# Kernel tuning notes

Measured on AMD Instinct MI355X. Metric: run time of the kernel, lower is better.

Reference implementation:

```python
import jax, jax.numpy as jnp
import numpy as np

S, B, HID, NH = 256, 2, 512, 8
HD = HID // NH
C = 1.0            # Poincare ball curvature c (geoopt k = -c)
SQC = C ** 0.5
EPS = 1e-15


def _artanh(x):
    return jnp.arctanh(jnp.clip(x, -1 + 1e-7, 1 - 1e-7))


def artan_k(x):
    return _artanh(SQC * x) / SQC


def tan_k(x):
    return jnp.tanh(SQC * x) / SQC


def mobius_add(x, y):
    x2 = jnp.sum(x * x, -1, keepdims=True)
    y2 = jnp.sum(y * y, -1, keepdims=True)
    xy = jnp.sum(x * y, -1, keepdims=True)
    num = (1 + 2 * C * xy + C * y2) * x + (1 - C * x2) * y
    den = 1 + 2 * C * xy + C * C * x2 * y2
    return num / jnp.maximum(den, EPS)


def mobius_matvec(W, x):
    x_norm = jnp.maximum(jnp.linalg.norm(x, axis=-1, keepdims=True), EPS)
    mx = x @ W.T
    mx_norm = jnp.maximum(jnp.linalg.norm(mx, axis=-1, keepdims=True), EPS)
    res = tan_k(mx_norm / x_norm * artan_k(x_norm)) * (mx / mx_norm)
    zero = jnp.all(mx == 0, axis=-1, keepdims=True)
    return jnp.where(zero, 0.0, res)


def projx(x):
    n = jnp.maximum(jnp.linalg.norm(x, axis=-1, keepdims=True), EPS)
    maxnorm = (1 - 4e-3) / SQC  # float32 eps in geoopt
    return jnp.where(n > maxnorm, x / n * maxnorm, x)


def expmap0(u):
    n = jnp.maximum(jnp.linalg.norm(u, axis=-1, keepdims=True), EPS)
    return tan_k(n) * u / n


def logmap0(y):
    n = jnp.maximum(jnp.linalg.norm(y, axis=-1, keepdims=True), EPS)
    return artan_k(n) * y / n


def mobius_scalar_mul(r, x):
    n = jnp.maximum(jnp.linalg.norm(x, axis=-1, keepdims=True), EPS)
    return tan_k(r * artan_k(n)) * x / n


def manifold_linear(W, b, x):
    return projx(mobius_add(mobius_matvec(W, x), b))


def setup_inputs() -> dict:
    key = jax.random.key(0)
    ks = jax.random.split(key, 7)
    q = jax.random.normal(ks[0], (S, B, HID), jnp.float32) * 0.02
    w = lambda k: jax.random.normal(k, (HID, HID), jnp.float32) * 0.02
    bias = lambda k: jax.random.normal(k, (HID,), jnp.float32) * 0.01
    return {"query": q,
            "Wq": w(ks[1]), "bq": bias(ks[2]),
            "Wk": w(ks[3]), "bk": bias(ks[4]),
            "Wv": w(ks[5]), "bv": bias(ks[6])}


def reference(query, Wq, bq, Wk, bk, Wv, bv):
    x = jnp.transpose(query, (1, 0, 2))  # [B,S,HID], key=value=query
    Bn, Sn, _ = x.shape
    q = manifold_linear(Wq, bq, x)
    k = manifold_linear(Wk, bk, x)
    v = manifold_linear(Wv, bv, x)
    # faithful to torch .view(-1, H, S, D): plain memory reshape (not transpose)
    ql = expmap0(logmap0(q).reshape(Bn, NH, Sn, HD))
    kl = expmap0(logmap0(k).reshape(Bn, NH, Sn, HD))
    vl = expmap0(logmap0(v).reshape(Bn, NH, Sn, HD))
    # pairwise mobius_add(-q, k) -> [B,H,Q,N,D]; torch norm(p=-2) over D (faithful)
    diff = mobius_add(-ql[:, :, :, None, :], kl[:, :, None, :, :])
    t1 = jnp.sum(jnp.maximum(diff * diff, 1e-30) ** -1.0, axis=-1) ** -0.5
    scores = jnp.clip(-2.0 * artan_k(t1), -1e10, 1e10)
    probs = jax.nn.sigmoid(scores)  # [B,H,Q,N]; dropout p=0 -> identity
    # weighted gyro-midpoint over N (geoopt _weighted_midpoint, reducedim=[-1])
    gamma = 2.0 / jnp.maximum(1.0 - C * jnp.sum(vl * vl, -1), EPS)  # [B,H,N]
    denom = jnp.einsum('bhqn,bhn->bhq', probs, gamma - 1.0)
    sgn = jnp.where(denom >= 0, 1.0, -1.0)
    denom = sgn * jnp.maximum(jnp.abs(denom), 1e-10)
    nom = jnp.einsum('bhqn,bhnd->bhqd', probs, gamma[..., None] * vl)
    ctx = mobius_scalar_mul(0.5, nom / denom[..., None])  # [B,H,Q,D]
    ctx = jnp.transpose(ctx, (0, 2, 1, 3))  # [B,Q,H,D]
    ctx = expmap0(logmap0(ctx).reshape(Bn, Sn, HID))
    return jnp.transpose(ctx, (1, 0, 2)), probs
```

## Files before the change

### kernel.cpp

```cpp
#include <hip/hip_runtime.h>
#include <math.h>

constexpr int S_   = 256;
constexpr int B_   = 2;
constexpr int HID_ = 512;
constexpr int NH_  = 8;
constexpr int HD_  = 64;
constexpr int BSH  = B_ * S_ * HID_;

__device__ __forceinline__ float artanh_c(float x) {
    x = fminf(fmaxf(x, -0.9999999f), 0.9999999f);
    return 0.5f * __logf((1.f + x) / (1.f - x));
}

__device__ __forceinline__ float wsum64(float v) {
    #pragma unroll
    for (int o = 1; o < 64; o <<= 1) v += __shfl_xor(v, o, 64);
    return v;
}

__device__ __forceinline__ float block_sum_256(float v, float* red) {
    const int t = threadIdx.x;
    __syncthreads();
    red[t] = v;
    __syncthreads();
    #pragma unroll
    for (int sft = 128; sft > 0; sft >>= 1) {
        if (t < sft) red[t] += red[t + sft];
        __syncthreads();
    }
    return red[0];
}

__global__ __launch_bounds__(256) void gemm3_kernel(
    const float* __restrict__ query,
    const float* __restrict__ Wq, const float* __restrict__ Wk,
    const float* __restrict__ Wv, float* __restrict__ ws_mx)
{
    const int tid   = threadIdx.x;
    const int which = blockIdx.x >> 8;
    const int tmp   = blockIdx.x & 255;
    const int row0  = (tmp >> 4) * 32;
    const int col0  = (tmp & 15) * 32;
    const float* __restrict__ W = (which == 0) ? Wq : (which == 1) ? Wk : Wv;
    float* __restrict__ outp = ws_mx + (size_t)which * (HID_ * HID_);

    __shared__ __align__(16) float sA[32][36];
    __shared__ __align__(16) float sB[32][36];

    const int sr = tid >> 3;
    const int sk = (tid & 7) * 4;
    const int gra = row0 + sr;
    const float* pa = query + (size_t)((gra & 255) * 2 + (gra >> 8)) * HID_ + sk;
    const float* pb = W + (size_t)(col0 + sr) * HID_ + sk;

    const int ty = tid >> 4, tx = tid & 15;
    float acc[2][2] = {};

    float4 va = *(const float4*)pa;
    float4 vb = *(const float4*)pb;
    for (int k0 = 0; k0 < HID_; k0 += 32) {
        __syncthreads();
        sA[sk+0][sr] = va.x; sA[sk+1][sr] = va.y; sA[sk+2][sr] = va.z; sA[sk+3][sr] = va.w;
        sB[sk+0][sr] = vb.x; sB[sk+1][sr] = vb.y; sB[sk+2][sr] = vb.z; sB[sk+3][sr] = vb.w;
        __syncthreads();
        if (k0 + 32 < HID_) {
            va = *(const float4*)(pa + k0 + 32);
            vb = *(const float4*)(pb + k0 + 32);
        }
        #pragma unroll
        for (int kk = 0; kk < 32; ++kk) {
            const float2 av = *(const float2*)&sA[kk][ty * 2];
            const float2 bv = *(const float2*)&sB[kk][tx * 2];
            acc[0][0] = fmaf(av.x, bv.x, acc[0][0]);
            acc[0][1] = fmaf(av.x, bv.y, acc[0][1]);
            acc[1][0] = fmaf(av.y, bv.x, acc[1][0]);
            acc[1][1] = fmaf(av.y, bv.y, acc[1][1]);
        }
    }
    #pragma unroll
    for (int i = 0; i < 2; ++i) {
        *(float2*)&outp[(size_t)(row0 + ty * 2 + i) * HID_ + col0 + tx * 2] =
            make_float2(acc[i][0], acc[i][1]);
    }
}

__global__ __launch_bounds__(256) void mobius_rows_kernel(
    const float* __restrict__ query,
    const float* __restrict__ bq, const float* __restrict__ bk,
    const float* __restrict__ bv,
    float* __restrict__ ws_qkv, float* __restrict__ ws_gamma)
{
    const int lane = threadIdx.x & 63;
    const int wv   = threadIdx.x >> 6;
    const int row  = blockIdx.x * 4 + wv;
    const int which = row >> 9;
    const int rr    = row & 511;
    const float* __restrict__ bias = (which == 0) ? bq : (which == 1) ? bk : bv;
    float* mrow = ws_qkv + (size_t)row * HID_;
    const float* xrow = query + (size_t)((rr & 255) * 2 + (rr >> 8)) * HID_;

    float m[8], x[8], bb[8];
    *(float4*)&m[0]  = ((const float4*)mrow)[lane * 2];
    *(float4*)&m[4]  = ((const float4*)mrow)[lane * 2 + 1];
    *(float4*)&x[0]  = ((const float4*)xrow)[lane * 2];
    *(float4*)&x[4]  = ((const float4*)xrow)[lane * 2 + 1];
    *(float4*)&bb[0] = ((const float4*)bias)[lane * 2];
    *(float4*)&bb[4] = ((const float4*)bias)[lane * 2 + 1];

    float x2p = 0.f, m2p = 0.f, b2p = 0.f;
    #pragma unroll
    for (int j = 0; j < 8; ++j) {
        x2p = fmaf(x[j], x[j], x2p);
        m2p = fmaf(m[j], m[j], m2p);
        b2p = fmaf(bb[j], bb[j], b2p);
    }
    const float x2s = wsum64(x2p);
    const float mn2 = wsum64(m2p);
    const float b2s = wsum64(b2p);
    const float xn = fmaxf(sqrtf(x2s), 1e-15f);
    const float mn = fmaxf(sqrtf(mn2), 1e-15f);
    const float fac = tanhf(mn / xn * artanh_c(xn)) / mn;
    float r[8];
    float r2p = 0.f, ryp = 0.f;
    #pragma unroll
    for (int j = 0; j < 8; ++j) {
        r[j] = fac * m[j];
        r2p = fmaf(r[j], r[j], r2p);
        ryp = fmaf(r[j], bb[j], ryp);
    }
    const float r2s = wsum64(r2p);
    const float ry  = wsum64(ryp);
    const float a_c = 1.f + 2.f * ry + b2s;
    const float b_c = 1.f - r2s;
    const float den = 1.f + 2.f * ry + r2s * b2s;
    const float inv_den = 1.f / fmaxf(den, 1e-15f);
    float h[8];
    float h2p = 0.f;
    #pragma unroll
    for (int j = 0; j < 8; ++j) {
        h[j] = (a_c * r[j] + b_c * bb[j]) * inv_den;
        h2p = fmaf(h[j], h[j], h2p);
    }
    const float h2s = wsum64(h2p);
    float hn = fmaxf(sqrtf(h2s), 1e-15f);
    float pf = 1.f;
    if (hn > 0.996f) { pf = 0.996f / hn; hn = 0.996f; }
    const float lf = artanh_c(hn) / hn * pf;
    float l[8];
    float l2p = 0.f;
    #pragma unroll
    for (int j = 0; j < 8; ++j) {
        l[j] = lf * h[j];
        l2p = fmaf(l[j], l[j], l2p);
    }
    float cs = l2p;
    cs += __shfl_xor(cs, 1, 64);
    cs += __shfl_xor(cs, 2, 64);
    cs += __shfl_xor(cs, 4, 64);
    const float cn = fmaxf(sqrtf(cs), 1e-15f);
    const float th = tanhf(cn);
    const float sc = th / cn;
    float o[8];
    #pragma unroll
    for (int j = 0; j < 8; ++j) o[j] = sc * l[j];
    ((float4*)mrow)[lane * 2]     = *(float4*)&o[0];
    ((float4*)mrow)[lane * 2 + 1] = *(float4*)&o[4];
    if (which == 2 && (lane & 7) == 0) {
        const int j = lane >> 3;
        ws_gamma[(size_t)rr * NH_ + j] = 2.f / fmaxf(1.f - th * th, 1e-15f);
    }
}

__global__ __launch_bounds__(256) void attn_kernel(
    const float* __restrict__ ws_qkv, const float* __restrict__ gamma,
    float* __restrict__ probs, float* __restrict__ lc)
{
    const int tid = threadIdx.x;
    const int bh  = blockIdx.x >> 5;
    const int q0  = (blockIdx.x & 31) * 8;
    const float* __restrict__ ql = ws_qkv + (size_t)bh * (S_ * HD_);
    const float* __restrict__ kl = ws_qkv + (size_t)BSH + (size_t)bh * (S_ * HD_);
    const float* __restrict__ vl = ws_qkv + (size_t)2 * BSH + (size_t)bh * (S_ * HD_);

    __shared__ __align__(16) float kS[128 * 64];
    __shared__ __align__(16) float qS[8 * 64];
    __shared__ __align__(16) float pS[8 * 256];
    __shared__ float gS[S_];
    __shared__ float k2S[128];
    __shared__ float nomP[4][8][64];
    __shared__ float dnS[8];

    gS[tid] = gamma[(size_t)bh * S_ + tid];
    if (tid < 128) ((float4*)qS)[tid] = ((const float4*)(ql + (size_t)q0 * 64))[tid];
    __syncthreads();

    const int q_l = tid >> 5;
    const int n_i = tid & 31;
    float qv[64];
    #pragma unroll
    for (int c = 0; c < 16; ++c)
        *(float4*)&qv[c * 4] = *(const float4*)&qS[q_l * 64 + c * 4];
    float q2 = 0.f;
    #pragma unroll
    for (int d = 0; d < 64; ++d) q2 = fmaf(qv[d], qv[d], q2);
    const float b_c = 1.f - q2;
    float* __restrict__ prow = probs + ((size_t)(bh * S_ + q0 + q_l)) * S_;

    const int c4 = tid & 15;
    const int nb = tid >> 4;
    float sp = 0.f, spg = 0.f;

    for (int half = 0; half < 2; ++half) {
        __syncthreads();
        #pragma unroll
        for (int jj = 0; jj < 8; ++jj) {
            const int n = nb + 16 * jj;
            const float4 v = *(const float4*)(kl + ((size_t)(half * 128 + n)) * 64 + c4 * 4);
            *(float4*)&kS[n * 64 + ((c4 ^ (n & 15)) * 4)] = v;
            float pk = fmaf(v.x, v.x, fmaf(v.y, v.y, fmaf(v.z, v.z, v.w * v.w)));
            pk += __shfl_xor(pk, 1, 64);
            pk += __shfl_xor(pk, 2, 64);
            pk += __shfl_xor(pk, 4, 64);
            pk += __shfl_xor(pk, 8, 64);
            if (c4 == 0) k2S[n] = pk;
        }
        __syncthreads();
        #pragma unroll
        for (int j = 0; j < 4; ++j) {
            const int n = n_i + 32 * j;
            float kv[64];
            #pragma unroll
            for (int c = 0; c < 16; ++c)
                *(float4*)&kv[c * 4] = *(const float4*)&kS[n * 64 + ((c ^ (n & 15)) * 4)];
            float s = 0.f;
            #pragma unroll
            for (int d = 0; d < 64; ++d) s = fmaf(qv[d], kv[d], s);
            const float k2  = k2S[n];
            const float a_c = 1.f - 2.f * s + k2;
            const float den = fmaxf(fmaf(q2, k2, 1.f - 2.f * s), 1e-15f);
            const float ra  = __builtin_amdgcn_rcpf(a_c);
            const float r_c = b_c * ra;
            const float scale = den * den * ra * ra;
            const float c2  = 1e-30f * scale;
            float invsum = 0.f;
            #pragma unroll
            for (int d = 0; d < 64; ++d) {
                const float w = fmaf(r_c, kv[d], -qv[d]);
                invsum += __builtin_amdgcn_rcpf(fmaf(w, w, c2));
            }
            const float t1 = __builtin_amdgcn_rsqf(scale * invsum);
            const float p = 0.5f - 0.5f * fminf(t1, 0.9999999f);
            const int gn = half * 128 + n;
            prow[gn] = p;
            const float g = gS[gn];
            pS[q_l * 256 + gn] = p * g;
            sp += p; spg += p * g;
        }
    }
    #pragma unroll
    for (int o = 1; o < 32; o <<= 1) {
        sp  += __shfl_xor(sp, o, 64);
        spg += __shfl_xor(spg, o, 64);
    }
    if ((tid & 31) == 0) dnS[q_l] = spg - sp;
    __syncthreads();

    const int w = tid >> 6, d = tid & 63;
    float acc[8] = {};
    const float* __restrict__ vbase = vl + (size_t)(w * 64) * 64;
    #pragma unroll 4
    for (int i4 = 0; i4 < 16; ++i4) {
        float vv[4];
        #pragma unroll
        for (int j2 = 0; j2 < 4; ++j2) vv[j2] = vbase[(size_t)(i4 * 4 + j2) * 64 + d];
        #pragma unroll
        for (int qq = 0; qq < 8; ++qq) {
            const float4 pq = *(const float4*)&pS[qq * 256 + w * 64 + i4 * 4];
            acc[qq] = fmaf(pq.x, vv[0], acc[qq]);
            acc[qq] = fmaf(pq.y, vv[1], acc[qq]);
            acc[qq] = fmaf(pq.z, vv[2], acc[qq]);
            acc[qq] = fmaf(pq.w, vv[3], acc[qq]);
        }
    }
    #pragma unroll
    for (int qq = 0; qq < 8; ++qq) nomP[w][qq][d] = acc[qq];
    __syncthreads();

    #pragma unroll
    for (int t = 0; t < 2; ++t) {
        const int qq = (tid >> 6) + 4 * t;
        const float nom = nomP[0][qq][d] + nomP[1][qq][d] + nomP[2][qq][d] + nomP[3][qq][d];
        const float dd = dnS[qq];
        const float adn = fmaxf(fabsf(dd), 1e-10f);
        const float sden = (dd >= 0.f) ? adn : -adn;
        const float m = nom / sden;
        const float ss = wsum64(m * m);
        const float nn = fmaxf(sqrtf(ss), 1e-15f);
        const float s1 = tanhf(0.5f * artanh_c(nn));
        const float res = s1 * m / nn;
        const float nres = fmaxf(s1, 1e-15f);
        lc[((size_t)(bh * S_ + q0 + qq)) * HD_ + d] = (artanh_c(nres) / nres) * res;
    }
}

__global__ __launch_bounds__(256) void outproj_kernel(
    const float* __restrict__ lc, float* __restrict__ out0)
{
    const int t = threadIdx.x;
    const int s = blockIdx.x & (S_ - 1);
    const int b = blockIdx.x >> 8;
    __shared__ float red[256];
    const int h0 = t >> 6, d0 = t & 63;
    const int e1 = t + 256;
    const int h1 = e1 >> 6, d1 = e1 & 63;
    const float v0 = lc[(((size_t)(b * NH_ + h0)) * S_ + s) * HD_ + d0];
    const float v1 = lc[(((size_t)(b * NH_ + h1)) * S_ + s) * HD_ + d1];
    const float ss = block_sum_256(v0 * v0 + v1 * v1, red);
    const float nn = fmaxf(sqrtf(ss), 1e-15f);
    const float f = tanhf(nn) / nn;
    float* orow = out0 + ((size_t)(s * B_ + b)) * HID_;
    orow[t] = f * v0;
    orow[t + 256] = f * v1;
}

extern "C" void kernel_launch(void* const* d_in, const int* in_sizes, int n_in,
                              void* d_out, int out_size, void* d_ws, size_t ws_size,
                              hipStream_t stream) {
    (void)in_sizes; (void)n_in; (void)out_size; (void)ws_size;
    const float* query = (const float*)d_in[0];
    const float* Wq = (const float*)d_in[1];
    const float* bq = (const float*)d_in[2];
    const float* Wk = (const float*)d_in[3];
    const float* bk = (const float*)d_in[4];
    const float* Wv = (const float*)d_in[5];
    const float* bv = (const float*)d_in[6];

    float* out0  = (float*)d_out;
    float* probs = out0 + (size_t)S_ * B_ * HID_;

    float* ws       = (float*)d_ws;
    float* ws_qkv   = ws;
    float* ws_gamma = ws + (size_t)3 * BSH;
    float* ws_lc    = ws + (size_t)3 * BSH + 4096;

    gemm3_kernel<<<dim3(768), dim3(256), 0, stream>>>(query, Wq, Wk, Wv, ws_qkv);
    mobius_rows_kernel<<<dim3(384), dim3(256), 0, stream>>>(query, bq, bk, bv, ws_qkv, ws_gamma);
    attn_kernel<<<dim3(512), dim3(256), 0, stream>>>(ws_qkv, ws_gamma, probs, ws_lc);
    outproj_kernel<<<dim3(B_ * S_), dim3(256), 0, stream>>>(ws_lc, out0);
}
```

Measured before the change: 129.0 us.

## Restructure QKV GEMM with wave-uniform A loads and swizzled W tile

Rewrites the projection GEMM so each block computes a 32x128 output tile. Each wave holds 8 rows whose query values are read straight from global memory as wave-uniform (broadcast) loads, and each lane computes two output columns from an XOR-swizzled shared-memory W tile. The aim is fewer, larger blocks with more work per thread and fewer shared-memory transactions. The costs are that A is no longer staged in LDS, so each k-step issues scalar or broadcast global loads, and only 192 blocks are launched, which may leave many CUs on the MI355X idle.

```diff
diff --git a/kernel.cpp b/kernel.cpp
--- a/kernel.cpp
+++ b/kernel.cpp
@@ -37,51 +37,65 @@
     const float* __restrict__ Wq, const float* __restrict__ Wk,
     const float* __restrict__ Wv, float* __restrict__ ws_mx)
 {
-    const int tid   = threadIdx.x;
-    const int which = blockIdx.x >> 8;
-    const int tmp   = blockIdx.x & 255;
-    const int row0  = (tmp >> 4) * 32;
-    const int col0  = (tmp & 15) * 32;
+    const int tid  = threadIdx.x;
+    const int lane = tid & 63;
+    const int wv   = __builtin_amdgcn_readfirstlane(tid >> 6);
+    const int rb   = blockIdx.x >> 2;
+    const int cb   = (blockIdx.x & 3) * 128;
+    const int which = (rb * 32) >> 9;
     const float* __restrict__ W = (which == 0) ? Wq : (which == 1) ? Wk : Wv;
-    float* __restrict__ outp = ws_mx + (size_t)which * (HID_ * HID_);
-
-    __shared__ __align__(16) float sA[32][36];
-    __shared__ __align__(16) float sB[32][36];
-
-    const int sr = tid >> 3;
-    const int sk = (tid & 7) * 4;
-    const int gra = row0 + sr;
-    const float* pa = query + (size_t)((gra & 255) * 2 + (gra >> 8)) * HID_ + sk;
-    const float* pb = W + (size_t)(col0 + sr) * HID_ + sk;
-
-    const int ty = tid >> 4, tx = tid & 15;
-    float acc[2][2] = {};
-
-    float4 va = *(const float4*)pa;
-    float4 vb = *(const float4*)pb;
+
+    const int rloc = (rb * 32) & 511;
+    const int wrow = rloc + wv * 8;
+    const float* xr[8];
+    #pragma unroll
+    for (int i = 0; i < 8; ++i) {
+        const int rr = wrow + i;
+        xr[i] = query + (size_t)((rr & 255) * 2 + (rr >> 8)) * HID_;
+    }
+
+    __shared__ __align__(16) float sB[128 * 32];
+
+    const int sc = tid >> 1;
+    const int sk = (tid & 1) * 16;
+    const float* wp = W + (size_t)(cb + sc) * HID_ + sk;
+    const int swz_st = (sc & 7) << 2;
+
+    float acc[8][2] = {};
+    float4 bvp[4];
+    #pragma unroll
+    for (int j = 0; j < 4; ++j) bvp[j] = *(const float4*)(wp + j * 4);
+
     for (int k0 = 0; k0 < HID_; k0 += 32) {
         __syncthreads();
-        sA[sk+0][sr] = va.x; sA[sk+1][sr] = va.y; sA[sk+2][sr] = va.z; sA[sk+3][sr] = va.w;
-        sB[sk+0][sr] = vb.x; sB[sk+1][sr] = vb.y; sB[sk+2][sr] = vb.z; sB[sk+3][sr] = vb.w;
+        #pragma unroll
+        for (int j = 0; j < 4; ++j)
+            *(float4*)&sB[(sc * 32 + sk + j * 4) ^ swz_st] = bvp[j];
         __syncthreads();
         if (k0 + 32 < HID_) {
-            va = *(const float4*)(pa + k0 + 32);
-            vb = *(const float4*)(pb + k0 + 32);
-        }
-        #pragma unroll
-        for (int kk = 0; kk < 32; ++kk) {
-            const float2 av = *(const float2*)&sA[kk][ty * 2];
-            const float2 bv = *(const float2*)&sB[kk][tx * 2];
-            acc[0][0] = fmaf(av.x, bv.x, acc[0][0]);
-            acc[0][1] = fmaf(av.x, bv.y, acc[0][1]);
-            acc[1][0] = fmaf(av.y, bv.x, acc[1][0]);
-            acc[1][1] = fmaf(av.y, bv.y, acc[1][1]);
-        }
-    }
-    #pragma unroll
-    for (int i = 0; i < 2; ++i) {
-        *(float2*)&outp[(size_t)(row0 + ty * 2 + i) * HID_ + col0 + tx * 2] =
-            make_float2(acc[i][0], acc[i][1]);
+            #pragma unroll
+            for (int j = 0; j < 4; ++j) bvp[j] = *(const float4*)(wp + k0 + 32 + j * 4);
+        }
+        #pragma unroll
+        for (int kk = 0; kk < 32; kk += 4) {
+            const int bidx = (lane * 32 + kk) ^ ((lane & 7) << 2);
+            const float4 b0 = *(const float4*)&sB[bidx];
+            const float4 b1 = *(const float4*)&sB[bidx + 2048];
+            #pragma unroll
+            for (int i = 0; i < 8; ++i) {
+                const float4 a = *(const float4*)(xr[i] + k0 + kk);
+                acc[i][0] = fmaf(a.w, b0.w, fmaf(a.z, b0.z,
+                            fmaf(a.y, b0.y, fmaf(a.x, b0.x, acc[i][0]))));
+                acc[i][1] = fmaf(a.w, b1.w, fmaf(a.z, b1.z,
+                            fmaf(a.y, b1.y, fmaf(a.x, b1.x, acc[i][1]))));
+            }
+        }
+    }
+    #pragma unroll
+    for (int i = 0; i < 8; ++i) {
+        const size_t gr = (size_t)(rb * 32 + wv * 8 + i);
+        ws_mx[gr * HID_ + cb + lane]      = acc[i][0];
+        ws_mx[gr * HID_ + cb + 64 + lane] = acc[i][1];
     }
 }
 
@@ -344,7 +358,7 @@
     float* ws_gamma = ws + (size_t)3 * BSH;
     float* ws_lc    = ws + (size_t)3 * BSH + 4096;
 
-    gemm3_kernel<<<dim3(768), dim3(256), 0, stream>>>(query, Wq, Wk, Wv, ws_qkv);
+    gemm3_kernel<<<dim3(192), dim3(256), 0, stream>>>(query, Wq, Wk, Wv, ws_qkv);
     mobius_rows_kernel<<<dim3(384), dim3(256), 0, stream>>>(query, bq, bk, bv, ws_qkv, ws_gamma);
     attn_kernel<<<dim3(512), dim3(256), 0, stream>>>(ws_qkv, ws_gamma, probs, ws_lc);
     outproj_kernel<<<dim3(B_ * S_), dim3(256), 0, stream>>>(ws_lc, out0);
```

Result: slower. 176.3 us (+36.7%).

## Replace FP32 SIMT QKV GEMM with split-bf16 MFMA GEMM plus conversion pass

Applied to the files above, without the earlier changes.

Adds a conversion kernel that splits the query and weight matrices into high and low bf16 halves. The three projection GEMMs then run on bf16 MFMA instructions, using three products (hi*hi, hi*lo, lo*hi) to approximate FP32 accuracy. LDS tiles use an XOR swizzle. The goal is to cut the cost of the scalar FMA GEMM, in exchange for an extra kernel launch, an extra global round trip for the converted operands, and slightly lower precision than true FP32.

```diff
diff --git a/kernel.cpp b/kernel.cpp
--- a/kernel.cpp
+++ b/kernel.cpp
@@ -8,6 +8,10 @@
 constexpr int HD_  = 64;
 constexpr int BSH  = B_ * S_ * HID_;
 
+typedef unsigned short u16;
+typedef short s16x8 __attribute__((ext_vector_type(8)));
+typedef float f32x4 __attribute__((ext_vector_type(4)));
+
 __device__ __forceinline__ float artanh_c(float x) {
     x = fminf(fmaxf(x, -0.9999999f), 0.9999999f);
     return 0.5f * __logf((1.f + x) / (1.f - x));
@@ -32,57 +36,129 @@
     return red[0];
 }
 
-__global__ __launch_bounds__(256) void gemm3_kernel(
-    const float* __restrict__ query,
-    const float* __restrict__ Wq, const float* __restrict__ Wk,
-    const float* __restrict__ Wv, float* __restrict__ ws_mx)
+__global__ __launch_bounds__(256) void cvt_kernel(
+    const float* __restrict__ query, const float* __restrict__ Wq,
+    const float* __restrict__ Wk, const float* __restrict__ Wv,
+    u16* __restrict__ Ahi, u16* __restrict__ Alo,
+    u16* __restrict__ Bhi, u16* __restrict__ Blo)
 {
-    const int tid   = threadIdx.x;
-    const int which = blockIdx.x >> 8;
-    const int tmp   = blockIdx.x & 255;
-    const int row0  = (tmp >> 4) * 32;
-    const int col0  = (tmp & 15) * 32;
-    const float* __restrict__ W = (which == 0) ? Wq : (which == 1) ? Wk : Wv;
-    float* __restrict__ outp = ws_mx + (size_t)which * (HID_ * HID_);
-
-    __shared__ __align__(16) float sA[32][36];
-    __shared__ __align__(16) float sB[32][36];
-
-    const int sr = tid >> 3;
-    const int sk = (tid & 7) * 4;
-    const int gra = row0 + sr;
-    const float* pa = query + (size_t)((gra & 255) * 2 + (gra >> 8)) * HID_ + sk;
-    const float* pb = W + (size_t)(col0 + sr) * HID_ + sk;
-
-    const int ty = tid >> 4, tx = tid & 15;
-    float acc[2][2] = {};
-
-    float4 va = *(const float4*)pa;
-    float4 vb = *(const float4*)pb;
+    const int lane = threadIdx.x & 63;
+    const int gr = blockIdx.x * 4 + (threadIdx.x >> 6);
+    const float* src;
+    u16 *dh, *dl;
+    if (gr < 512) {
+        src = query + (size_t)((gr & 255) * 2 + (gr >> 8)) * HID_;
+        dh = Ahi + (size_t)gr * HID_;
+        dl = Alo + (size_t)gr * HID_;
+    } else {
+        const int m = gr - 512;
+        const float* __restrict__ W = ((m >> 9) == 0) ? Wq : ((m >> 9) == 1) ? Wk : Wv;
+        src = W + (size_t)(m & 511) * HID_;
+        dh = Bhi + (size_t)m * HID_;
+        dl = Blo + (size_t)m * HID_;
+    }
+    float v[8];
+    *(float4*)&v[0] = *(const float4*)(src + lane * 8);
+    *(float4*)&v[4] = *(const float4*)(src + lane * 8 + 4);
+    s16x8 hv, lv;
+    #pragma unroll
+    for (int j = 0; j < 8; ++j) {
+        const unsigned u = __float_as_uint(v[j]);
+        const float hf = __uint_as_float(u & 0xFFFF0000u);
+        hv[j] = (short)(u >> 16);
+        lv[j] = (short)(__float_as_uint(v[j] - hf) >> 16);
+    }
+    *(s16x8*)(dh + lane * 8) = hv;
+    *(s16x8*)(dl + lane * 8) = lv;
+}
+
+__global__ __launch_bounds__(256) void gemm3_mfma_kernel(
+    const u16* __restrict__ Ahi, const u16* __restrict__ Alo,
+    const u16* __restrict__ Bhi, const u16* __restrict__ Blo,
+    float* __restrict__ ws_mx)
+{
+    const int tid = threadIdx.x;
+    const int rt = blockIdx.x >> 3;
+    const int ct = blockIdx.x & 7;
+    const int rloc  = (rt & 7) * 64;
+    const int brow0 = (rt >> 3) * 512 + ct * 64;
+
+    __shared__ __align__(16) u16 sAh[64 * 32];
+    __shared__ __align__(16) u16 sAl[64 * 32];
+    __shared__ __align__(16) u16 sBh[64 * 32];
+    __shared__ __align__(16) u16 sBl[64 * 32];
+
+    const int r = tid >> 2, s = tid & 3;
+    const u16* gAh = Ahi + (size_t)(rloc + r) * HID_ + s * 8;
+    const u16* gAl = Alo + (size_t)(rloc + r) * HID_ + s * 8;
+    const u16* gBh = Bhi + (size_t)(brow0 + r) * HID_ + s * 8;
+    const u16* gBl = Blo + (size_t)(brow0 + r) * HID_ + s * 8;
+    const int wslot = r * 32 + ((s ^ ((r >> 1) & 3)) * 8);
+
+    const int lane = tid & 63, w = tid >> 6;
+    const int wr = w >> 1, wc = w & 1;
+    const int fr = lane & 15;
+    const int fs = lane >> 4;
+    int aslot[2], bslot[2];
+    #pragma unroll
+    for (int i = 0; i < 2; ++i) {
+        const int ar = wr * 32 + i * 16 + fr;
+        aslot[i] = ar * 32 + ((fs ^ ((ar >> 1) & 3)) * 8);
+        const int br = wc * 32 + i * 16 + fr;
+        bslot[i] = br * 32 + ((fs ^ ((br >> 1) & 3)) * 8);
+    }
+
+    f32x4 acc[2][2];
+    #pragma unroll
+    for (int i = 0; i < 2; ++i)
+        #pragma unroll
+        for (int j = 0; j < 2; ++j) acc[i][j] = (f32x4){0.f, 0.f, 0.f, 0.f};
+
+    s16x8 pf0 = *(const s16x8*)gAh;
+    s16x8 pf1 = *(const s16x8*)gAl;
+    s16x8 pf2 = *(const s16x8*)gBh;
+    s16x8 pf3 = *(const s16x8*)gBl;
+
     for (int k0 = 0; k0 < HID_; k0 += 32) {
         __syncthreads();
-        sA[sk+0][sr] = va.x; sA[sk+1][sr] = va.y; sA[sk+2][sr] = va.z; sA[sk+3][sr] = va.w;
-        sB[sk+0][sr] = vb.x; sB[sk+1][sr] = vb.y; sB[sk+2][sr] = vb.z; sB[sk+3][sr] = vb.w;
+        *(s16x8*)&sAh[wslot] = pf0;
+        *(s16x8*)&sAl[wslot] = pf1;
+        *(s16x8*)&sBh[wslot] = pf2;
+        *(s16x8*)&sBl[wslot] = pf3;
         __syncthreads();
         if (k0 + 32 < HID_) {
-            va = *(const float4*)(pa + k0 + 32);
-            vb = *(const float4*)(pb + k0 + 32);
+            pf0 = *(const s16x8*)(gAh + k0 + 32);
+            pf1 = *(const s16x8*)(gAl + k0 + 32);
+            pf2 = *(const s16x8*)(gBh + k0 + 32);
+            pf3 = *(const s16x8*)(gBl + k0 + 32);
         }
-        #pragma unroll
-        for (int kk = 0; kk < 32; ++kk) {
-            const float2 av = *(const float2*)&sA[kk][ty * 2];
-            const float2 bv = *(const float2*)&sB[kk][tx * 2];
-            acc[0][0] = fmaf(av.x, bv.x, acc[0][0]);
-            acc[0][1] = fmaf(av.x, bv.y, acc[0][1]);
-            acc[1][0] = fmaf(av.y, bv.x, acc[1][0]);
-            acc[1][1] = fmaf(av.y, bv.y, acc[1][1]);
+        s16x8 ah[2], al[2], bh[2], bl[2];
+        #pragma unroll
+        for (int i = 0; i < 2; ++i) {
+            ah[i] = *(const s16x8*)&sAh[aslot[i]];
+            al[i] = *(const s16x8*)&sAl[aslot[i]];
+            bh[i] = *(const s16x8*)&sBh[bslot[i]];
+            bl[i] = *(const s16x8*)&sBl[bslot[i]];
         }
-    }
-    #pragma unroll
-    for (int i = 0; i < 2; ++i) {
-        *(float2*)&outp[(size_t)(row0 + ty * 2 + i) * HID_ + col0 + tx * 2] =
-            make_float2(acc[i][0], acc[i][1]);
-    }
+        #pragma unroll
+        for (int i = 0; i < 2; ++i)
+            #pragma unroll
+            for (int j = 0; j < 2; ++j) {
+                acc[i][j] = __builtin_amdgcn_mfma_f32_16x16x32_bf16(ah[i], bh[j], acc[i][j], 0, 0, 0);
+                acc[i][j] = __builtin_amdgcn_mfma_f32_16x16x32_bf16(ah[i], bl[j], acc[i][j], 0, 0, 0);
+                acc[i][j] = __builtin_amdgcn_mfma_f32_16x16x32_bf16(al[i], bh[j], acc[i][j], 0, 0, 0);
+            }
+    }
+    #pragma unroll
+    for (int i = 0; i < 2; ++i)
+        #pragma unroll
+        for (int j = 0; j < 2; ++j)
+            #pragma unroll
+            for (int q = 0; q < 4; ++q) {
+                const int row = rt * 64 + wr * 32 + i * 16 + fs * 4 + q;
+                const int col = ct * 64 + wc * 32 + j * 16 + fr;
+                ws_mx[(size_t)row * HID_ + col] = acc[i][j][q];
+            }
 }
 
 __global__ __launch_bounds__(256) void mobius_rows_kernel(
@@ -343,8 +419,13 @@
     float* ws_qkv   = ws;
     float* ws_gamma = ws + (size_t)3 * BSH;
     float* ws_lc    = ws + (size_t)3 * BSH + 4096;
-
-    gemm3_kernel<<<dim3(768), dim3(256), 0, stream>>>(query, Wq, Wk, Wv, ws_qkv);
+    u16* Ahi = (u16*)(ws + (size_t)3 * BSH + 4096 + 131072);
+    u16* Alo = Ahi + (size_t)512 * HID_;
+    u16* Bhi = Alo + (size_t)512 * HID_;
+    u16* Blo = Bhi + (size_t)1536 * HID_;
+
+    cvt_kernel<<<dim3(512), dim3(256), 0, stream>>>(query, Wq, Wk, Wv, Ahi, Alo, Bhi, Blo);
+    gemm3_mfma_kernel<<<dim3(192), dim3(256), 0, stream>>>(Ahi, Alo, Bhi, Blo, ws_qkv);
     mobius_rows_kernel<<<dim3(384), dim3(256), 0, stream>>>(query, bq, bk, bv, ws_qkv, ws_gamma);
     attn_kernel<<<dim3(512), dim3(256), 0, stream>>>(ws_qkv, ws_gamma, probs, ws_lc);
     outproj_kernel<<<dim3(B_ * S_), dim3(256), 0, stream>>>(ws_lc, out0);
```

After: 110.7 us. 1.16x faster.

## Use split-bf16 MFMA for the QKV projection GEMM with swizzled double-buffered LDS

Applied to the files above, without the earlier changes.

Replaces the scalar FP32 FMA tiled GEMM for the three projections with a matrix-core version. Each fp32 operand is split into bf16 hi and lo parts, and three MFMA 16x16x32 products (hh, hl, lh) are accumulated to approximate fp32 accuracy. The kernel also uses 32x64 tiles with XOR-swizzled double-buffered LDS and register prefetch. This trades some precision (the lo*lo term is dropped) and extra split work for much higher matrix throughput, and it halves the block count.

```diff
diff --git a/kernel.cpp b/kernel.cpp
--- a/kernel.cpp
+++ b/kernel.cpp
@@ -8,6 +8,10 @@
 constexpr int HD_  = 64;
 constexpr int BSH  = B_ * S_ * HID_;
 
+typedef unsigned short u16;
+typedef short s16x8 __attribute__((ext_vector_type(8)));
+typedef float f32x4 __attribute__((ext_vector_type(4)));
+
 __device__ __forceinline__ float artanh_c(float x) {
     x = fminf(fmaxf(x, -0.9999999f), 0.9999999f);
     return 0.5f * __logf((1.f + x) / (1.f - x));
@@ -32,57 +36,103 @@
     return red[0];
 }
 
-__global__ __launch_bounds__(256) void gemm3_kernel(
+__device__ __forceinline__ void split8(const float* v, s16x8& hi, s16x8& lo) {
+    #pragma unroll
+    for (int j = 0; j < 8; ++j) {
+        const unsigned u = __float_as_uint(v[j]);
+        const float hf = __uint_as_float(u & 0xFFFF0000u);
+        hi[j] = (short)(u >> 16);
+        lo[j] = (short)(__float_as_uint(v[j] - hf) >> 16);
+    }
+}
+
+__global__ __launch_bounds__(256) void gemm3_fused_kernel(
     const float* __restrict__ query,
     const float* __restrict__ Wq, const float* __restrict__ Wk,
     const float* __restrict__ Wv, float* __restrict__ ws_mx)
 {
-    const int tid   = threadIdx.x;
-    const int which = blockIdx.x >> 8;
-    const int tmp   = blockIdx.x & 255;
-    const int row0  = (tmp >> 4) * 32;
-    const int col0  = (tmp & 15) * 32;
+    const int tid = threadIdx.x;
+    const int rt = blockIdx.x >> 3;
+    const int ct = blockIdx.x & 7;
+    const int which = (rt * 32) >> 9;
+    const int rloc  = (rt * 32) & 511;
     const float* __restrict__ W = (which == 0) ? Wq : (which == 1) ? Wk : Wv;
-    float* __restrict__ outp = ws_mx + (size_t)which * (HID_ * HID_);
-
-    __shared__ __align__(16) float sA[32][36];
-    __shared__ __align__(16) float sB[32][36];
-
-    const int sr = tid >> 3;
-    const int sk = (tid & 7) * 4;
-    const int gra = row0 + sr;
-    const float* pa = query + (size_t)((gra & 255) * 2 + (gra >> 8)) * HID_ + sk;
-    const float* pb = W + (size_t)(col0 + sr) * HID_ + sk;
-
-    const int ty = tid >> 4, tx = tid & 15;
-    float acc[2][2] = {};
-
-    float4 va = *(const float4*)pa;
-    float4 vb = *(const float4*)pb;
-    for (int k0 = 0; k0 < HID_; k0 += 32) {
+
+    __shared__ __align__(16) u16 sA[2][2][32 * 64];
+    __shared__ __align__(16) u16 sB[2][2][64 * 64];
+
+    const int ra = tid >> 3, sa = tid & 7;
+    const int rb = tid >> 2, hb = (tid & 3) * 2;
+    const int axrow = rloc + ra;
+    const float* gA = query + (size_t)((axrow & 255) * 2 + (axrow >> 8)) * HID_ + sa * 8;
+    const float* gB = W + (size_t)(ct * 64 + rb) * HID_ + hb * 8;
+    const int wA  = ra * 64 + ((sa ^ (ra & 7)) * 8);
+    const int wB0 = rb * 64 + ((hb ^ (rb & 7)) * 8);
+    const int wB1 = rb * 64 + (((hb + 1) ^ (rb & 7)) * 8);
+
+    const int lane = tid & 63, wv = tid >> 6;
+    const int fr = lane & 15, fs = lane >> 4;
+    const int aB0 = fr * 64,        ax0 = fr & 7;
+    const int aB1 = (16 + fr) * 64, ax1 = (16 + fr) & 7;
+    const int bB  = (wv * 16 + fr) * 64, bx = (wv * 16 + fr) & 7;
+
+    float a8[8], b16[16];
+    f32x4 acc[2] = {(f32x4){0.f,0.f,0.f,0.f}, (f32x4){0.f,0.f,0.f,0.f}};
+
+#define G3_LOAD(c)  do { \
+        const int k0 = (c) * 64; \
+        *(float4*)&a8[0]  = *(const float4*)(gA + k0); \
+        *(float4*)&a8[4]  = *(const float4*)(gA + k0 + 4); \
+        *(float4*)&b16[0] = *(const float4*)(gB + k0); \
+        *(float4*)&b16[4] = *(const float4*)(gB + k0 + 4); \
+        *(float4*)&b16[8] = *(const float4*)(gB + k0 + 8); \
+        *(float4*)&b16[12]= *(const float4*)(gB + k0 + 12); \
+    } while (0)
+
+#define G3_WRITE(b) do { \
+        s16x8 h_, l_; \
+        split8(a8, h_, l_); \
+        *(s16x8*)&sA[b][0][wA] = h_;  *(s16x8*)&sA[b][1][wA] = l_; \
+        split8(&b16[0], h_, l_); \
+        *(s16x8*)&sB[b][0][wB0] = h_; *(s16x8*)&sB[b][1][wB0] = l_; \
+        split8(&b16[8], h_, l_); \
+        *(s16x8*)&sB[b][0][wB1] = h_; *(s16x8*)&sB[b][1][wB1] = l_; \
+    } while (0)
+
+    G3_LOAD(0);
+    G3_WRITE(0);
+
+    for (int c = 0; c < 8; ++c) {
+        const int p = c & 1;
         __syncthreads();
-        sA[sk+0][sr] = va.x; sA[sk+1][sr] = va.y; sA[sk+2][sr] = va.z; sA[sk+3][sr] = va.w;
-        sB[sk+0][sr] = vb.x; sB[sk+1][sr] = vb.y; sB[sk+2][sr] = vb.z; sB[sk+3][sr] = vb.w;
-        __syncthreads();
-        if (k0 + 32 < HID_) {
-            va = *(const float4*)(pa + k0 + 32);
-            vb = *(const float4*)(pb + k0 + 32);
+        if (c < 7) G3_LOAD(c + 1);
+        #pragma unroll
+        for (int h = 0; h < 2; ++h) {
+            const int sl = h * 4 + fs;
+            s16x8 ah0 = *(const s16x8*)&sA[p][0][aB0 + ((sl ^ ax0) * 8)];
+            s16x8 al0 = *(const s16x8*)&sA[p][1][aB0 + ((sl ^ ax0) * 8)];
+            s16x8 ah1 = *(const s16x8*)&sA[p][0][aB1 + ((sl ^ ax1) * 8)];
+            s16x8 al1 = *(const s16x8*)&sA[p][1][aB1 + ((sl ^ ax1) * 8)];
+            s16x8 bh  = *(const s16x8*)&sB[p][0][bB  + ((sl ^ bx)  * 8)];
+            s16x8 bl  = *(const s16x8*)&sB[p][1][bB  + ((sl ^ bx)  * 8)];
+            acc[0] = __builtin_amdgcn_mfma_f32_16x16x32_bf16(ah0, bh, acc[0], 0, 0, 0);
+            acc[0] = __builtin_amdgcn_mfma_f32_16x16x32_bf16(ah0, bl, acc[0], 0, 0, 0);
+            acc[0] = __builtin_amdgcn_mfma_f32_16x16x32_bf16(al0, bh, acc[0], 0, 0, 0);
+            acc[1] = __builtin_amdgcn_mfma_f32_16x16x32_bf16(ah1, bh, acc[1], 0, 0, 0);
+            acc[1] = __builtin_amdgcn_mfma_f32_16x16x32_bf16(ah1, bl, acc[1], 0, 0, 0);
+            acc[1] = __builtin_amdgcn_mfma_f32_16x16x32_bf16(al1, bh, acc[1], 0, 0, 0);
         }
-        #pragma unroll
-        for (int kk = 0; kk < 32; ++kk) {
-            const float2 av = *(const float2*)&sA[kk][ty * 2];
-            const float2 bv = *(const float2*)&sB[kk][tx * 2];
-            acc[0][0] = fmaf(av.x, bv.x, acc[0][0]);
-            acc[0][1] = fmaf(av.x, bv.y, acc[0][1]);
-            acc[1][0] = fmaf(av.y, bv.x, acc[1][0]);
-            acc[1][1] = fmaf(av.y, bv.y, acc[1][1]);
-        }
-    }
-    #pragma unroll
-    for (int i = 0; i < 2; ++i) {
-        *(float2*)&outp[(size_t)(row0 + ty * 2 + i) * HID_ + col0 + tx * 2] =
-            make_float2(acc[i][0], acc[i][1]);
-    }
+        if (c < 7) G3_WRITE((c + 1) & 1);
+    }
+#undef G3_LOAD
+#undef G3_WRITE
+
+    #pragma unroll
+    for (int i = 0; i < 2; ++i)
+        #pragma unroll
+        for (int q = 0; q < 4; ++q)
+            ws_mx[(size_t)(rt * 32 + i * 16 + fs * 4 + q) * HID_ + ct * 64 + wv * 16 + fr]
+                = acc[i][q];
 }
 
 __global__ __launch_bounds__(256) void mobius_rows_kernel(
@@ -344,7 +394,7 @@
     float* ws_gamma = ws + (size_t)3 * BSH;
     float* ws_lc    = ws + (size_t)3 * BSH + 4096;
 
-    gemm3_kernel<<<dim3(768), dim3(256), 0, stream>>>(query, Wq, Wk, Wv, ws_qkv);
+    gemm3_fused_kernel<<<dim3(384), dim3(256), 0, stream>>>(query, Wq, Wk, Wv, ws_qkv);
     mobius_rows_kernel<<<dim3(384), dim3(256), 0, stream>>>(query, bq, bk, bv, ws_qkv, ws_gamma);
     attn_kernel<<<dim3(512), dim3(256), 0, stream>>>(ws_qkv, ws_gamma, probs, ws_lc);
     outproj_kernel<<<dim3(B_ * S_), dim3(256), 0, stream>>>(ws_lc, out0);
```

Measured after the change: 108.8 us. 1.18x faster.
